# Kernel tuning notes

Hardware: AMD Instinct MI355X
Metric: run time of the kernel (lower is better)

The kernel has to match this reference:

```python
import jax, jax.numpy as jnp
import numpy as np

N = 4194304          # flat pixel batch (~2 full 1080p frames)
NUM_CAMERAS = 8
NUM_FRAMES = 1000
EPS = 1e-6


def setup_inputs() -> dict:
    key = jax.random.key(0)
    ks = jax.random.split(key, 8)
    W, H = 1920, 1080
    exposure_params = 0.2 * jax.random.normal(ks[0], (NUM_FRAMES,), jnp.float32)
    vignetting_params = 0.05 * jax.random.normal(ks[1], (NUM_CAMERAS, 3, 5), jnp.float32)
    color_params = 0.05 * jax.random.normal(ks[2], (NUM_FRAMES, 8), jnp.float32)
    # CRF raw init matching the module: softplus-inverse of 1.0 with minima (0.3,0.3,0.1), offset 0
    def _sp_inv(x, m):
        return float(np.log(np.expm1(max(1e-5, x - m))))
    crf0 = jnp.array([_sp_inv(1.0, 0.3), _sp_inv(1.0, 0.3), _sp_inv(1.0, 0.1), 0.0], jnp.float32)
    crf_params = (jnp.broadcast_to(crf0, (NUM_CAMERAS, 3, 4))
                  + 0.05 * jax.random.normal(ks[3], (NUM_CAMERAS, 3, 4), jnp.float32))
    rgb = jax.random.uniform(ks[4], (N, 3), jnp.float32)
    pixel_coords = jax.random.uniform(ks[5], (N, 2), jnp.float32) * jnp.array([W, H], jnp.float32)
    camera_idcs = jax.random.randint(ks[6], (N,), 0, NUM_CAMERAS, jnp.int32)
    frame_idcs = jax.random.randint(ks[7], (N,), 0, NUM_FRAMES, jnp.int32)
    return dict(exposure_params=exposure_params, vignetting_params=vignetting_params,
                color_params=color_params, crf_params=crf_params, rgb=rgb,
                pixel_coords=pixel_coords, camera_idcs=camera_idcs, frame_idcs=frame_idcs,
                resolution_w=W, resolution_h=H)


def _ppisp(exposure_params, vignetting_params, color_params, crf_params,
           rgb, pixel_coords, camera_idcs, frame_idcs, resolution_w, resolution_h):
    # 1) per-frame exposure (EV scale)
    exp_scale = jnp.exp2(exposure_params[frame_idcs])[:, None]            # [N,1]
    x = rgb * exp_scale                                                    # [N,3]

    # 2) per-camera, per-channel radial vignetting: params = [cx, cy, a1, a2, a3]
    vig = vignetting_params[camera_idcs]                                   # [N,3,5]
    u = pixel_coords[:, 0] / jnp.float32(resolution_w) - 0.5               # [N]
    v = pixel_coords[:, 1] / jnp.float32(resolution_h) - 0.5               # [N]
    du = u[:, None] - vig[..., 0]                                          # [N,3]
    dv = v[:, None] - vig[..., 1]
    r2 = du * du + dv * dv                                                 # [N,3]
    falloff = 1.0 + r2 * (vig[..., 2] + r2 * (vig[..., 3] + r2 * vig[..., 4]))
    x = x * falloff

    # 3) per-frame color: WB gains (r,b) + off-diagonal 3x3 mixing matrix (8 params)
    cp = color_params[frame_idcs]                                          # [N,8]
    gains = jnp.stack([jnp.exp(cp[:, 0]), jnp.ones_like(cp[:, 0]), jnp.exp(cp[:, 1])], axis=-1)
    x = x * gains
    one = jnp.ones_like(cp[:, 0])
    M = jnp.stack([
        jnp.stack([one,      cp[:, 2], cp[:, 3]], axis=-1),
        jnp.stack([cp[:, 4], one,      cp[:, 5]], axis=-1),
        jnp.stack([cp[:, 6], cp[:, 7], one     ], axis=-1)], axis=-2)      # [N,3,3]
    x = jnp.einsum('nij,nj->ni', M, x)

    # 4) per-camera, per-channel 4-param sigmoid CRF, identity at init
    crf = crf_params[camera_idcs]                                          # [N,3,4]
    a = jax.nn.softplus(crf[..., 0]) + 0.3
    b = jax.nn.softplus(crf[..., 1]) + 0.3
    c = jax.nn.softplus(crf[..., 2]) + 0.1
    d = crf[..., 3]
    xc = jnp.clip(x, EPS, 1.0)
    xa = xc ** a
    out = xa / (xa + (c * (1.0 - xc) + EPS) ** b) + d                      # [N,3]
    return out


def reference(exposure_params, vignetting_params, color_params, crf_params,
              rgb, pixel_coords, camera_idcs, frame_idcs, resolution_w, resolution_h):
    return _ppisp(exposure_params, vignetting_params, color_params, crf_params,
                  rgb, pixel_coords, camera_idcs, frame_idcs, resolution_w, resolution_h)
```

## Files before the change

kernel.cpp:

```cpp
#include <hip/hip_runtime.h>


__device__ __forceinline__ unsigned bf16r(float x) {
    unsigned b = __float_as_uint(x);
    return (b + 0x7fffu + ((b >> 16) & 1u)) >> 16;
}
__device__ __forceinline__ unsigned packbf(float lo, float hi) {
    return bf16r(lo) | (bf16r(hi) << 16);
}
__device__ __forceinline__ float ulo(unsigned u) { return __uint_as_float(u << 16); }
__device__ __forceinline__ float uhi(unsigned u) { return __uint_as_float(u & 0xffff0000u); }

__global__ __launch_bounds__(1024, 4) void ppisp_main(
    const float*  __restrict__ expo,
    const float*  __restrict__ vigp,
    const float4* __restrict__ colorp4,
    const float*  __restrict__ crfp,
    const float4* __restrict__ rgb4,
    const float4* __restrict__ pc4,
    const int4*   __restrict__ cam4,
    const int4*   __restrict__ frm4,
    const int*    __restrict__ resw,
    const int*    __restrict__ resh,
    float4* __restrict__ out4,
    int ngroups, int groups_per_block, int num_frames, int ncam)
{
    __shared__ uint4 sA[1000];
    __shared__ float sB[1000];
    __shared__ float scamf[224];

    int tid = threadIdx.x;
    for (int f = tid; f < num_frames; f += 1024) {
        float e = exp2f(expo[f]);
        float4 c0 = colorp4[f * 2 + 0];
        float4 c1 = colorp4[f * 2 + 1];
        float g_r = e * expf(c0.x);
        float g_b = e * expf(c0.y);
        uint4 A;
        A.x = packbf(g_r, e);
        A.y = packbf(g_b, c0.z);
        A.z = packbf(c0.w, c1.x);
        A.w = packbf(c1.y, c1.z);
        sA[f] = A;
        sB[f] = c1.w;
    }
    if (tid < ncam * 3) {
        int c = tid / 3, ch = tid % 3;
        const float* vp = vigp + tid * 5;
        const float* cf = crfp + tid * 4;
        float* r = scamf + c * 28 + ch * 9;
        r[0] = vp[0];
        r[1] = vp[1];
        r[2] = vp[2];
        r[3] = vp[3];
        r[4] = vp[4];
        r[5] = log1pf(expf(cf[0])) + 0.3f;
        r[6] = log1pf(expf(cf[1])) + 0.3f;
        r[7] = log1pf(expf(cf[2])) + 0.1f;
        r[8] = cf[3];
        if (ch == 0) scamf[c * 28 + 27] = 0.f;
    }
    __syncthreads();

    const float4* scam4 = (const float4*)scamf;
    float invW = 1.0f / (float)resw[0];
    float invH = 1.0f / (float)resh[0];

    int gbase = blockIdx.x * groups_per_block;
    int gend = gbase + groups_per_block;
    if (gend > ngroups) gend = ngroups;

    for (int g = gbase + tid; g < gend; g += 1024) {
        float4 r0  = rgb4[(size_t)g * 3 + 0];
        float4 r1  = rgb4[(size_t)g * 3 + 1];
        float4 r2v = rgb4[(size_t)g * 3 + 2];
        float4 p0  = pc4[(size_t)g * 2 + 0];
        float4 p1  = pc4[(size_t)g * 2 + 1];
        int4 cams = cam4[g];
        int4 frms = frm4[g];

        float rgbp[4][3] = {{r0.x, r0.y, r0.z},
                            {r0.w, r1.x, r1.y},
                            {r1.z, r1.w, r2v.x},
                            {r2v.y, r2v.z, r2v.w}};
        float px[4] = {p0.x, p0.z, p1.x, p1.z};
        float py[4] = {p0.y, p0.w, p1.y, p1.w};
        int camA[4] = {cams.x, cams.y, cams.z, cams.w};
        int frmA[4] = {frms.x, frms.y, frms.z, frms.w};

        float o[12];

#pragma unroll
        for (int p = 0; p < 4; ++p) {
            uint4 A = sA[frmA[p]];
            float m21 = sB[frmA[p]];
            float g_r = ulo(A.x), g_g = uhi(A.x);
            float g_b = ulo(A.y), m01 = uhi(A.y);
            float m02 = ulo(A.z), m10 = uhi(A.z);
            float m12 = ulo(A.w), m20 = uhi(A.w);

            int cb = camA[p] * 7;
            float4 q0 = scam4[cb + 0];
            float4 q1 = scam4[cb + 1];
            float4 q2 = scam4[cb + 2];
            float4 q3 = scam4[cb + 3];
            float4 q4 = scam4[cb + 4];
            float4 q5 = scam4[cb + 5];
            float4 q6 = scam4[cb + 6];

            float u = px[p] * invW - 0.5f;
            float v = py[p] * invH - 0.5f;

            float cx0 = q0.x, cy0 = q0.y, a10 = q0.z, a20 = q0.w, a30 = q1.x;
            float aa0 = q1.y, bb0 = q1.z, cc0 = q1.w, dd0 = q2.x;
            float cx1 = q2.y, cy1 = q2.z, a11 = q2.w, a21 = q3.x, a31 = q3.y;
            float aa1 = q3.z, bb1 = q3.w, cc1 = q4.x, dd1 = q4.y;
            float cx2 = q4.z, cy2 = q4.w, a12 = q5.x, a22 = q5.y, a32 = q5.z;
            float aa2 = q5.w, bb2 = q6.x, cc2 = q6.y, dd2 = q6.z;

            float du0 = u - cx0, dv0 = v - cy0;
            float du1 = u - cx1, dv1 = v - cy1;
            float du2 = u - cx2, dv2 = v - cy2;
            float r20 = du0 * du0 + dv0 * dv0;
            float r21 = du1 * du1 + dv1 * dv1;
            float r22 = du2 * du2 + dv2 * dv2;
            float fa0 = 1.0f + r20 * (a10 + r20 * (a20 + r20 * a30));
            float fa1 = 1.0f + r21 * (a11 + r21 * (a21 + r21 * a31));
            float fa2 = 1.0f + r22 * (a12 + r22 * (a22 + r22 * a32));

            float x0 = rgbp[p][0] * g_r * fa0;
            float x1 = rgbp[p][1] * g_g * fa1;
            float x2 = rgbp[p][2] * g_b * fa2;

            float y0 = x0 + m01 * x1 + m02 * x2;
            float y1 = m10 * x0 + x1 + m12 * x2;
            float y2 = m20 * x0 + m21 * x1 + x2;

            float xc0 = fminf(fmaxf(y0, 1e-6f), 1.0f);
            float xc1 = fminf(fmaxf(y1, 1e-6f), 1.0f);
            float xc2 = fminf(fmaxf(y2, 1e-6f), 1.0f);

            float xa0 = __builtin_amdgcn_exp2f(aa0 * __builtin_amdgcn_logf(xc0));
            float xa1 = __builtin_amdgcn_exp2f(aa1 * __builtin_amdgcn_logf(xc1));
            float xa2 = __builtin_amdgcn_exp2f(aa2 * __builtin_amdgcn_logf(xc2));
            float t0 = cc0 * (1.0f - xc0) + 1e-6f;
            float t1 = cc1 * (1.0f - xc1) + 1e-6f;
            float t2 = cc2 * (1.0f - xc2) + 1e-6f;
            float tb0 = __builtin_amdgcn_exp2f(bb0 * __builtin_amdgcn_logf(t0));
            float tb1 = __builtin_amdgcn_exp2f(bb1 * __builtin_amdgcn_logf(t1));
            float tb2 = __builtin_amdgcn_exp2f(bb2 * __builtin_amdgcn_logf(t2));

            o[p * 3 + 0] = xa0 * __builtin_amdgcn_rcpf(xa0 + tb0) + dd0;
            o[p * 3 + 1] = xa1 * __builtin_amdgcn_rcpf(xa1 + tb1) + dd1;
            o[p * 3 + 2] = xa2 * __builtin_amdgcn_rcpf(xa2 + tb2) + dd2;
        }

        out4[(size_t)g * 3 + 0] = make_float4(o[0], o[1], o[2], o[3]);
        out4[(size_t)g * 3 + 1] = make_float4(o[4], o[5], o[6], o[7]);
        out4[(size_t)g * 3 + 2] = make_float4(o[8], o[9], o[10], o[11]);
    }
}

extern "C" void kernel_launch(void* const* d_in, const int* in_sizes, int n_in,
                              void* d_out, int out_size, void* d_ws, size_t ws_size,
                              hipStream_t stream) {
    const float* expo   = (const float*)d_in[0];
    const float* vigp   = (const float*)d_in[1];
    const float* colorp = (const float*)d_in[2];
    const float* crfp   = (const float*)d_in[3];
    const float* rgb    = (const float*)d_in[4];
    const float* pc     = (const float*)d_in[5];
    const int*   cam    = (const int*)d_in[6];
    const int*   frm    = (const int*)d_in[7];
    const int*   rw     = (const int*)d_in[8];
    const int*   rh     = (const int*)d_in[9];

    int num_frames = in_sizes[0];
    int ncam = in_sizes[1] / 15;
    int N = in_sizes[4] / 3;

    int ngroups = N / 4;
    int blocks = 512;
    int groups_per_block = (ngroups + blocks - 1) / blocks;
    ppisp_main<<<blocks, 1024, 0, stream>>>(
        expo, vigp, (const float4*)colorp, crfp,
        (const float4*)rgb, (const float4*)pc, (const int4*)cam, (const int4*)frm,
        rw, rh, (float4*)d_out,
        ngroups, groups_per_block, num_frames, ncam);
}
```

Before: 182.1 us.

## Split table precompute into pre-kernel, prefetch next group, use 2-pixel groups

```diff
diff --git a/kernel.cpp b/kernel.cpp
--- a/kernel.cpp
+++ b/kernel.cpp
@@ -10,59 +10,140 @@
 }
 __device__ __forceinline__ float ulo(unsigned u) { return __uint_as_float(u << 16); }
 __device__ __forceinline__ float uhi(unsigned u) { return __uint_as_float(u & 0xffff0000u); }
-
-__global__ __launch_bounds__(1024, 4) void ppisp_main(
-    const float*  __restrict__ expo,
-    const float*  __restrict__ vigp,
-    const float4* __restrict__ colorp4,
-    const float*  __restrict__ crfp,
-    const float4* __restrict__ rgb4,
-    const float4* __restrict__ pc4,
-    const int4*   __restrict__ cam4,
-    const int4*   __restrict__ frm4,
-    const int*    __restrict__ resw,
-    const int*    __restrict__ resh,
-    float4* __restrict__ out4,
-    int ngroups, int groups_per_block, int num_frames, int ncam)
-{
-    __shared__ uint4 sA[1000];
-    __shared__ float sB[1000];
-    __shared__ float scamf[224];
-
-    int tid = threadIdx.x;
-    for (int f = tid; f < num_frames; f += 1024) {
-        float e = exp2f(expo[f]);
-        float4 c0 = colorp4[f * 2 + 0];
-        float4 c1 = colorp4[f * 2 + 1];
-        float g_r = e * expf(c0.x);
-        float g_b = e * expf(c0.y);
+__device__ __forceinline__ float ush(unsigned short s) { return __uint_as_float(((unsigned)s) << 16); }
+
+__global__ void ppisp_pre(const float* __restrict__ expo,
+                          const float* __restrict__ colorp,
+                          const float* __restrict__ vigp,
+                          const float* __restrict__ crfp,
+                          uint4* __restrict__ wsA,
+                          float* __restrict__ wsCam,
+                          unsigned short* __restrict__ wsB,
+                          int num_frames, int ncam) {
+    int tid = blockIdx.x * blockDim.x + threadIdx.x;
+    if (tid < num_frames) {
+        float e = exp2f(expo[tid]);
+        const float* cp = colorp + tid * 8;
+        float g_r = e * expf(cp[0]);
+        float g_b = e * expf(cp[1]);
         uint4 A;
         A.x = packbf(g_r, e);
-        A.y = packbf(g_b, c0.z);
-        A.z = packbf(c0.w, c1.x);
-        A.w = packbf(c1.y, c1.z);
-        sA[f] = A;
-        sB[f] = c1.w;
+        A.y = packbf(g_b, cp[2]);
+        A.z = packbf(cp[3], cp[4]);
+        A.w = packbf(cp[5], cp[6]);
+        wsA[tid] = A;
+        wsB[tid] = (unsigned short)bf16r(cp[7]);
     }
     if (tid < ncam * 3) {
         int c = tid / 3, ch = tid % 3;
         const float* vp = vigp + tid * 5;
         const float* cf = crfp + tid * 4;
-        float* r = scamf + c * 28 + ch * 9;
-        r[0] = vp[0];
-        r[1] = vp[1];
-        r[2] = vp[2];
-        r[3] = vp[3];
-        r[4] = vp[4];
+        float* r = wsCam + c * 28 + ch * 9;
+        r[0] = vp[0]; r[1] = vp[1]; r[2] = vp[2]; r[3] = vp[3]; r[4] = vp[4];
         r[5] = log1pf(expf(cf[0])) + 0.3f;
         r[6] = log1pf(expf(cf[1])) + 0.3f;
         r[7] = log1pf(expf(cf[2])) + 0.1f;
         r[8] = cf[3];
-        if (ch == 0) scamf[c * 28 + 27] = 0.f;
+        if (ch == 0) wsCam[c * 28 + 27] = 0.f;
     }
+}
+
+__device__ __forceinline__ void px_compute(
+    float rr, float gg, float bb, float pxx, float pyy, int camI, int frmI,
+    float invW, float invH,
+    const uint4* __restrict__ sA, const unsigned short* __restrict__ sB,
+    const float4* __restrict__ scam4,
+    float& o0, float& o1, float& o2)
+{
+    uint4 A = sA[frmI];
+    float m21 = ush(sB[frmI]);
+    float g_r = ulo(A.x), g_g = uhi(A.x);
+    float g_b = ulo(A.y), m01 = uhi(A.y);
+    float m02 = ulo(A.z), m10 = uhi(A.z);
+    float m12 = ulo(A.w), m20 = uhi(A.w);
+
+    int cb = camI * 7;
+    float4 q0 = scam4[cb + 0];
+    float4 q1 = scam4[cb + 1];
+    float4 q2 = scam4[cb + 2];
+    float4 q3 = scam4[cb + 3];
+    float4 q4 = scam4[cb + 4];
+    float4 q5 = scam4[cb + 5];
+    float4 q6 = scam4[cb + 6];
+
+    float u = pxx * invW - 0.5f;
+    float v = pyy * invH - 0.5f;
+
+    float cx0 = q0.x, cy0 = q0.y, a10 = q0.z, a20 = q0.w, a30 = q1.x;
+    float aa0 = q1.y, bb0 = q1.z, cc0 = q1.w, dd0 = q2.x;
+    float cx1 = q2.y, cy1 = q2.z, a11 = q2.w, a21 = q3.x, a31 = q3.y;
+    float aa1 = q3.z, bb1 = q3.w, cc1 = q4.x, dd1 = q4.y;
+    float cx2 = q4.z, cy2 = q4.w, a12 = q5.x, a22 = q5.y, a32 = q5.z;
+    float aa2 = q5.w, bb2 = q6.x, cc2 = q6.y, dd2 = q6.z;
+
+    float du0 = u - cx0, dv0 = v - cy0;
+    float du1 = u - cx1, dv1 = v - cy1;
+    float du2 = u - cx2, dv2 = v - cy2;
+    float r20 = du0 * du0 + dv0 * dv0;
+    float r21 = du1 * du1 + dv1 * dv1;
+    float r22 = du2 * du2 + dv2 * dv2;
+    float fa0 = 1.0f + r20 * (a10 + r20 * (a20 + r20 * a30));
+    float fa1 = 1.0f + r21 * (a11 + r21 * (a21 + r21 * a31));
+    float fa2 = 1.0f + r22 * (a12 + r22 * (a22 + r22 * a32));
+
+    float x0 = rr * g_r * fa0;
+    float x1 = gg * g_g * fa1;
+    float x2 = bb * g_b * fa2;
+
+    float y0 = x0 + m01 * x1 + m02 * x2;
+    float y1 = m10 * x0 + x1 + m12 * x2;
+    float y2 = m20 * x0 + m21 * x1 + x2;
+
+    float xc0 = fminf(fmaxf(y0, 1e-6f), 1.0f);
+    float xc1 = fminf(fmaxf(y1, 1e-6f), 1.0f);
+    float xc2 = fminf(fmaxf(y2, 1e-6f), 1.0f);
+
+    float lx0 = __builtin_amdgcn_logf(xc0);
+    float lx1 = __builtin_amdgcn_logf(xc1);
+    float lx2 = __builtin_amdgcn_logf(xc2);
+    float t0 = cc0 * (1.0f - xc0) + 1e-6f;
+    float t1 = cc1 * (1.0f - xc1) + 1e-6f;
+    float t2 = cc2 * (1.0f - xc2) + 1e-6f;
+    float lt0 = __builtin_amdgcn_logf(t0);
+    float lt1 = __builtin_amdgcn_logf(t1);
+    float lt2 = __builtin_amdgcn_logf(t2);
+    float z0 = bb0 * lt0 - aa0 * lx0;
+    float z1 = bb1 * lt1 - aa1 * lx1;
+    float z2 = bb2 * lt2 - aa2 * lx2;
+    o0 = __builtin_amdgcn_rcpf(1.0f + __builtin_amdgcn_exp2f(z0)) + dd0;
+    o1 = __builtin_amdgcn_rcpf(1.0f + __builtin_amdgcn_exp2f(z1)) + dd1;
+    o2 = __builtin_amdgcn_rcpf(1.0f + __builtin_amdgcn_exp2f(z2)) + dd2;
+}
+
+__global__ __launch_bounds__(256, 4) void ppisp_main(
+    const uint4*  __restrict__ wsA,
+    const float4* __restrict__ wsCam4,
+    const unsigned* __restrict__ wsBu,
+    const float2* __restrict__ rgb2,
+    const float4* __restrict__ pc4,
+    const int2*   __restrict__ cam2,
+    const int2*   __restrict__ frm2,
+    const int*    __restrict__ resw,
+    const int*    __restrict__ resh,
+    float2* __restrict__ out2,
+    int ngroups, int groups_per_block, int num_frames, int ncam)
+{
+    __shared__ uint4 sA[1000];
+    __shared__ float4 scam4s[56];
+    __shared__ unsigned sBu[500];
+
+    int tid = threadIdx.x;
+    for (int i = tid; i < 1000; i += 256) sA[i] = wsA[i];
+    if (tid < 56) scam4s[tid] = wsCam4[tid];
+    for (int i = tid; i < 500; i += 256) sBu[i] = wsBu[i];
     __syncthreads();
 
-    const float4* scam4 = (const float4*)scamf;
+    const unsigned short* sB = (const unsigned short*)sBu;
     float invW = 1.0f / (float)resw[0];
     float invH = 1.0f / (float)resh[0];
 
@@ -70,94 +151,45 @@
     int gend = gbase + groups_per_block;
     if (gend > ngroups) gend = ngroups;
 
-    for (int g = gbase + tid; g < gend; g += 1024) {
-        float4 r0  = rgb4[(size_t)g * 3 + 0];
-        float4 r1  = rgb4[(size_t)g * 3 + 1];
-        float4 r2v = rgb4[(size_t)g * 3 + 2];
-        float4 p0  = pc4[(size_t)g * 2 + 0];
-        float4 p1  = pc4[(size_t)g * 2 + 1];
-        int4 cams = cam4[g];
-        int4 frms = frm4[g];
-
-        float rgbp[4][3] = {{r0.x, r0.y, r0.z},
-                            {r0.w, r1.x, r1.y},
-                            {r1.z, r1.w, r2v.x},
-                            {r2v.y, r2v.z, r2v.w}};
-        float px[4] = {p0.x, p0.z, p1.x, p1.z};
-        float py[4] = {p0.y, p0.w, p1.y, p1.w};
-        int camA[4] = {cams.x, cams.y, cams.z, cams.w};
-        int frmA[4] = {frms.x, frms.y, frms.z, frms.w};
-
-        float o[12];
-
-#pragma unroll
-        for (int p = 0; p < 4; ++p) {
-            uint4 A = sA[frmA[p]];
-            float m21 = sB[frmA[p]];
-            float g_r = ulo(A.x), g_g = uhi(A.x);
-            float g_b = ulo(A.y), m01 = uhi(A.y);
-            float m02 = ulo(A.z), m10 = uhi(A.z);
-            float m12 = ulo(A.w), m20 = uhi(A.w);
-
-            int cb = camA[p] * 7;
-            float4 q0 = scam4[cb + 0];
-            float4 q1 = scam4[cb + 1];
-            float4 q2 = scam4[cb + 2];
-            float4 q3 = scam4[cb + 3];
-            float4 q4 = scam4[cb + 4];
-            float4 q5 = scam4[cb + 5];
-            float4 q6 = scam4[cb + 6];
-
-            float u = px[p] * invW - 0.5f;
-            float v = py[p] * invH - 0.5f;
-
-            float cx0 = q0.x, cy0 = q0.y, a10 = q0.z, a20 = q0.w, a30 = q1.x;
-            float aa0 = q1.y, bb0 = q1.z, cc0 = q1.w, dd0 = q2.x;
-            float cx1 = q2.y, cy1 = q2.z, a11 = q2.w, a21 = q3.x, a31 = q3.y;
-            float aa1 = q3.z, bb1 = q3.w, cc1 = q4.x, dd1 = q4.y;
-            float cx2 = q4.z, cy2 = q4.w, a12 = q5.x, a22 = q5.y, a32 = q5.z;
-            float aa2 = q5.w, bb2 = q6.x, cc2 = q6.y, dd2 = q6.z;
-
-            float du0 = u - cx0, dv0 = v - cy0;
-            float du1 = u - cx1, dv1 = v - cy1;
-            float du2 = u - cx2, dv2 = v - cy2;
-            float r20 = du0 * du0 + dv0 * dv0;
-            float r21 = du1 * du1 + dv1 * dv1;
-            float r22 = du2 * du2 + dv2 * dv2;
-            float fa0 = 1.0f + r20 * (a10 + r20 * (a20 + r20 * a30));
-            float fa1 = 1.0f + r21 * (a11 + r21 * (a21 + r21 * a31));
-            float fa2 = 1.0f + r22 * (a12 + r22 * (a22 + r22 * a32));
-
-            float x0 = rgbp[p][0] * g_r * fa0;
-            float x1 = rgbp[p][1] * g_g * fa1;
-            float x2 = rgbp[p][2] * g_b * fa2;
-
-            float y0 = x0 + m01 * x1 + m02 * x2;
-            float y1 = m10 * x0 + x1 + m12 * x2;
-            float y2 = m20 * x0 + m21 * x1 + x2;
-
-            float xc0 = fminf(fmaxf(y0, 1e-6f), 1.0f);
-            float xc1 = fminf(fmaxf(y1, 1e-6f), 1.0f);
-            float xc2 = fminf(fmaxf(y2, 1e-6f), 1.0f);
-
-            float xa0 = __builtin_amdgcn_exp2f(aa0 * __builtin_amdgcn_logf(xc0));
-            float xa1 = __builtin_amdgcn_exp2f(aa1 * __builtin_amdgcn_logf(xc1));
-            float xa2 = __builtin_amdgcn_exp2f(aa2 * __builtin_amdgcn_logf(xc2));
-            float t0 = cc0 * (1.0f - xc0) + 1e-6f;
-            float t1 = cc1 * (1.0f - xc1) + 1e-6f;
-            float t2 = cc2 * (1.0f - xc2) + 1e-6f;
-            float tb0 = __builtin_amdgcn_exp2f(bb0 * __builtin_amdgcn_logf(t0));
-            float tb1 = __builtin_amdgcn_exp2f(bb1 * __builtin_amdgcn_logf(t1));
-            float tb2 = __builtin_amdgcn_exp2f(bb2 * __builtin_amdgcn_logf(t2));
-
-            o[p * 3 + 0] = xa0 * __builtin_amdgcn_rcpf(xa0 + tb0) + dd0;
-            o[p * 3 + 1] = xa1 * __builtin_amdgcn_rcpf(xa1 + tb1) + dd1;
-            o[p * 3 + 2] = xa2 * __builtin_amdgcn_rcpf(xa2 + tb2) + dd2;
+    int g = gbase + tid;
+    if (g >= gend) return;
+
+    float2 a0 = rgb2[(size_t)g * 3 + 0];
+    float2 a1 = rgb2[(size_t)g * 3 + 1];
+    float2 a2 = rgb2[(size_t)g * 3 + 2];
+    float4 P  = pc4[g];
+    int2 cams = cam2[g];
+    int2 frms = frm2[g];
+
+    while (true) {
+        int gn = g + 256;
+        bool more = gn < gend;
+        float2 na0, na1, na2;
+        float4 nP;
+        int2 ncams, nfrms;
+        if (more) {
+            na0 = rgb2[(size_t)gn * 3 + 0];
+            na1 = rgb2[(size_t)gn * 3 + 1];
+            na2 = rgb2[(size_t)gn * 3 + 2];
+            nP  = pc4[gn];
+            ncams = cam2[gn];
+            nfrms = frm2[gn];
         }
 
-        out4[(size_t)g * 3 + 0] = make_float4(o[0], o[1], o[2], o[3]);
-        out4[(size_t)g * 3 + 1] = make_float4(o[4], o[5], o[6], o[7]);
-        out4[(size_t)g * 3 + 2] = make_float4(o[8], o[9], o[10], o[11]);
+        float o00, o01, o02, o10, o11, o12;
+        px_compute(a0.x, a0.y, a1.x, P.x, P.y, cams.x, frms.x,
+                   invW, invH, sA, sB, scam4s, o00, o01, o02);
+        px_compute(a1.y, a2.x, a2.y, P.z, P.w, cams.y, frms.y,
+                   invW, invH, sA, sB, scam4s, o10, o11, o12);
+
+        out2[(size_t)g * 3 + 0] = make_float2(o00, o01);
+        out2[(size_t)g * 3 + 1] = make_float2(o02, o10);
+        out2[(size_t)g * 3 + 2] = make_float2(o11, o12);
+
+        if (!more) break;
+        g = gn;
+        a0 = na0; a1 = na1; a2 = na2;
+        P = nP; cams = ncams; frms = nfrms;
     }
 }
 
@@ -179,12 +211,22 @@
     int ncam = in_sizes[1] / 15;
     int N = in_sizes[4] / 3;
 
-    int ngroups = N / 4;
-    int blocks = 512;
+    uint4* wsA = (uint4*)d_ws;
+    float* wsCam = (float*)((char*)d_ws + 16000);
+    unsigned short* wsB = (unsigned short*)((char*)d_ws + 16896);
+
+    int pre_threads = 256;
+    int pre_blocks = (num_frames + pre_threads - 1) / pre_threads;
+    if (pre_blocks < 1) pre_blocks = 1;
+    ppisp_pre<<<pre_blocks, pre_threads, 0, stream>>>(
+        expo, colorp, vigp, crfp, wsA, wsCam, wsB, num_frames, ncam);
+
+    int ngroups = N / 2;
+    int blocks = 2048;
     int groups_per_block = (ngroups + blocks - 1) / blocks;
-    ppisp_main<<<blocks, 1024, 0, stream>>>(
-        expo, vigp, (const float4*)colorp, crfp,
-        (const float4*)rgb, (const float4*)pc, (const int4*)cam, (const int4*)frm,
-        rw, rh, (float4*)d_out,
+    ppisp_main<<<blocks, 256, 0, stream>>>(
+        wsA, (const float4*)wsCam, (const unsigned*)wsB,
+        (const float2*)rgb, (const float4*)pc, (const int2*)cam, (const int2*)frm,
+        rw, rh, (float2*)d_out,
         ngroups, groups_per_block, num_frames, ncam);
 }
```

New measurement: 180.6 us. Within noise of the previous version (-0.8%).
